# Kernel tuning notes

Hardware: AMD Instinct MI355X
Metric: run time of the kernel (lower is better)

Reference implementation:

```python
import jax, jax.numpy as jnp
import numpy as np
from jax import lax

# Static config (matches init_kwargs)
D_MODEL = 1024
EXPAND = 2
D_INNER = D_MODEL * EXPAND          # 2048
HEAD_DIM = 64
N_HEADS = D_INNER // HEAD_DIM       # 32
N_GROUPS = 1
D_STATE = 128
D_CONV = 4
CONV_DIM = D_INNER + 2 * N_GROUPS * D_STATE        # 2304
D_IN_PROJ = 2 * D_INNER + 2 * N_GROUPS * D_STATE + N_HEADS  # 4384
SEQLEN = 8192
LN_EPS = 1e-5


def setup_inputs() -> dict:
    key = jax.random.key(0)
    ks = jax.random.split(key, 6)
    x = jax.random.normal(ks[0], (SEQLEN, D_MODEL), jnp.float32)
    W_in = jax.random.normal(ks[1], (D_IN_PROJ, D_MODEL), jnp.float32) / np.sqrt(D_MODEL)
    W_conv = jax.random.normal(ks[2], (CONV_DIM, 1, D_CONV), jnp.float32) / np.sqrt(D_CONV)
    b_conv = jnp.zeros((CONV_DIM,), jnp.float32)
    # dt_bias init per Mamba2: dt ~ LogUniform(dt_min, dt_max), inverse-softplus
    dt = jnp.exp(jax.random.uniform(ks[3], (N_HEADS,)) * (np.log(0.1) - np.log(0.001)) + np.log(0.001))
    dt = jnp.clip(dt, 1e-4)
    dt_bias = dt + jnp.log(-jnp.expm1(-dt))
    A_log = jnp.log(jax.random.uniform(ks[4], (N_HEADS,), minval=1.0, maxval=16.0))
    D_param = jnp.ones((N_HEADS,), jnp.float32)
    ln_w = jnp.ones((D_INNER,), jnp.float32)
    ln_b = jnp.zeros((D_INNER,), jnp.float32)
    W_out = jax.random.normal(ks[5], (D_MODEL, D_INNER), jnp.float32) / np.sqrt(D_INNER)
    return dict(x=x, W_in=W_in, W_conv=W_conv, b_conv=b_conv, dt_bias=dt_bias,
                A_log=A_log, D_param=D_param, ln_w=ln_w, ln_b=ln_b, W_out=W_out)


def reference(x, W_in, W_conv, b_conv, dt_bias, A_log, D_param, ln_w, ln_b, W_out):
    L = x.shape[0]
    zxbcdt = x @ W_in.T                                   # (L, d_in_proj)
    z = zxbcdt[:, :D_INNER]                               # gate
    xbc = zxbcdt[:, D_INNER:D_INNER + CONV_DIM]           # (L, conv_dim)
    dt = jax.nn.softplus(zxbcdt[:, D_INNER + CONV_DIM:] + dt_bias)  # (L, h)
    # depthwise causal-window conv with SAME padding over the sequence
    lhs = xbc.T[None]                                      # (1, conv_dim, L)
    conv = lax.conv_general_dilated(lhs, W_conv, (1,), 'SAME',
                                    feature_group_count=CONV_DIM,
                                    dimension_numbers=('NCH', 'OIH', 'NCH'))[0]
    xbc = jax.nn.silu((conv + b_conv[:, None]).T)          # (L, conv_dim)
    x_ssm = xbc[:, :D_INNER].reshape(L, N_HEADS, HEAD_DIM)
    B = xbc[:, D_INNER:D_INNER + N_GROUPS * D_STATE].reshape(L, N_GROUPS, D_STATE)
    C = xbc[:, D_INNER + N_GROUPS * D_STATE:].reshape(L, N_GROUPS, D_STATE)
    hpg = N_HEADS // N_GROUPS
    Bh = jnp.repeat(B, hpg, axis=1)                        # (L, h, n)
    Ch = jnp.repeat(C, hpg, axis=1)                        # (L, h, n)
    A = -jnp.exp(A_log)                                    # (h,), negative
    a = jnp.exp(dt * A)                                    # (L, h) per-token decay in (0,1)
    V = x_ssm * dt[..., None]                              # discretized input (L, h, p)
    # non-causal SSD (VSSD): global state H then readout, plus D skip
    H = jnp.einsum('lhn,lh,lhp->hnp', Bh, a, V)            # (h, n, p)
    y = jnp.einsum('lhn,hnp->lhp', Ch, H) + D_param[None, :, None] * x_ssm
    y = y.reshape(L, D_INNER)
    # LayerNorm (eqx default: weight+bias, eps=1e-5), then gate by z
    mu = jnp.mean(y, axis=-1, keepdims=True)
    var = jnp.var(y, axis=-1, keepdims=True)
    y = ((y - mu) / jnp.sqrt(var + LN_EPS)) * ln_w + ln_b
    y = y * z
    return y @ W_out.T                                     # (L, d_model)
```

## Files before the change

kernel.cpp:

```cpp
#include <hip/hip_runtime.h>
#include <hip/hip_bf16.h>
#include <math.h>

#define L_SEQ 8192
#define DM 1024
#define DI 2048
#define NH 32
#define HD 64
#define DS 128
#define CDIM 2304
#define DPROJ 4384
#define NPAD_IN 4608
#define KSPLIT 16
#define OPROWS 2176

typedef short bf16x8 __attribute__((ext_vector_type(8)));
typedef float floatx4 __attribute__((ext_vector_type(4)));
typedef unsigned short u16x4 __attribute__((ext_vector_type(4)));
typedef unsigned short u16x8 __attribute__((ext_vector_type(8)));

#define AS1(p) ((const __attribute__((address_space(1))) void*)(p))
#define AS3(p) ((__attribute__((address_space(3))) void*)(p))

__device__ __forceinline__ float bf2f(unsigned short u) {
  union { unsigned int i; float f; } c; c.i = ((unsigned int)u) << 16; return c.f;
}
__device__ __forceinline__ unsigned short f2bf(float f) {
  return __bfloat16_as_ushort(__float2bfloat16(f));
}

template <int OMODE>
__global__ __launch_bounds__(512, 4)
void gemm128_tlp(const unsigned short* __restrict__ A, int lda,
                 const unsigned short* __restrict__ B, int ldb,
                 void* __restrict__ Cout, int ldc,
                 int K, int Nstore) {
  __shared__ __align__(16) char lds[65536];
  const int t = threadIdx.x;
  const int lane = t & 63;
  const int w = t >> 6;
  const int wm = w & 1, wn = w >> 1;
  const int fr = lane & 15, quad = lane >> 4;

  int gx = gridDim.x, gy = gridDim.y;
  int linear = blockIdx.y * gx + blockIdx.x;
  int xcd = linear & 7, loc = linear >> 3;
  int mper = gy >> 3;
  int mt = xcd * mper + loc % mper;
  int nt = loc / mper;
  const int m0 = mt << 7, n0 = nt << 7;
  const int NT = K >> 6;

  floatx4 acc[4][2];
#pragma unroll
  for (int i = 0; i < 4; ++i)
#pragma unroll
    for (int j = 0; j < 2; ++j) acc[i][j] = (floatx4){0.f, 0.f, 0.f, 0.f};
  bf16x8 af[4][2], b0[2], b1[2];

  auto stA = [&](int buf, int kt) {
#pragma unroll
    for (int i = 0; i < 2; ++i) {
      int o = (i * 512 + t) * 16;
      int os = o ^ (((o >> 7) & 7) << 4);
      int rloc = os >> 7, kb = os & 127;
      const unsigned short* src = A + (size_t)(m0 + rloc) * lda + (kt << 6) + (kb >> 1);
      __builtin_amdgcn_global_load_lds(AS1(src), AS3(lds + buf * 16384 + o), 16, 0, 0);
    }
  };
  auto stB = [&](int buf, int kt) {
#pragma unroll
    for (int i = 0; i < 2; ++i) {
      int o = (i * 512 + t) * 16;
      int os = o ^ (((o >> 7) & 7) << 4);
      int rloc = os >> 7, kb = os & 127;
      const unsigned short* src = B + (size_t)(n0 + rloc) * ldb + (kt << 6) + (kb >> 1);
      __builtin_amdgcn_global_load_lds(AS1(src),
          AS3(lds + 32768 + buf * 16384 + o), 16, 0, 0);
    }
  };
  auto rdA = [&](int buf, int mi, int ks) -> bf16x8 {
    int rloc = (wm << 6) | (mi << 4) | fr;
    return *(const bf16x8*)(lds + buf * 16384 + rloc * 128 +
                            (((ks << 6) | (quad << 4)) ^ ((fr & 7) << 4)));
  };
  auto rdB = [&](int buf, int ni, int ks) -> bf16x8 {
    int rloc = (wn << 5) | (ni << 4) | fr;
    return *(const bf16x8*)(lds + 32768 + buf * 16384 + rloc * 128 +
                            (((ks << 6) | (quad << 4)) ^ ((fr & 7) << 4)));
  };

  stA(0, 0); stB(0, 0);
  if (NT > 1) {
    stA(1, 1);
    asm volatile("s_waitcnt vmcnt(2)" ::: "memory");
  } else {
    asm volatile("s_waitcnt vmcnt(0)" ::: "memory");
  }
  __builtin_amdgcn_s_barrier();

  for (int kt = 0; kt < NT; ++kt) {
    const int buf = kt & 1;
    const bool pfB = (kt + 1 < NT);
    const bool pfA = (kt + 2 < NT);
#pragma unroll
    for (int mi = 0; mi < 4; ++mi) { af[mi][0] = rdA(buf, mi, 0); af[mi][1] = rdA(buf, mi, 1); }
    b0[0] = rdB(buf, 0, 0); b0[1] = rdB(buf, 0, 1);
    if (pfB) stB(buf ^ 1, kt + 1);
    __builtin_amdgcn_s_barrier();
    asm volatile("s_waitcnt lgkmcnt(0)" ::: "memory");
    __builtin_amdgcn_s_setprio(1);
#pragma unroll
    for (int mi = 0; mi < 4; ++mi)
#pragma unroll
      for (int ks = 0; ks < 2; ++ks)
        acc[mi][0] = __builtin_amdgcn_mfma_f32_16x16x32_bf16(af[mi][ks], b0[ks], acc[mi][0], 0, 0, 0);
    __builtin_amdgcn_s_setprio(0);
    __builtin_amdgcn_s_barrier();
    b1[0] = rdB(buf, 1, 0); b1[1] = rdB(buf, 1, 1);
    if (pfA) stA(buf, kt + 2);
    __builtin_amdgcn_s_barrier();
    asm volatile("s_waitcnt lgkmcnt(0)" ::: "memory");
    __builtin_amdgcn_s_setprio(1);
#pragma unroll
    for (int mi = 0; mi < 4; ++mi)
#pragma unroll
      for (int ks = 0; ks < 2; ++ks)
        acc[mi][1] = __builtin_amdgcn_mfma_f32_16x16x32_bf16(af[mi][ks], b1[ks], acc[mi][1], 0, 0, 0);
    __builtin_amdgcn_s_setprio(0);
    if (kt < NT - 1) {
      if (pfA) asm volatile("s_waitcnt vmcnt(2)" ::: "memory");
      else     asm volatile("s_waitcnt vmcnt(0)" ::: "memory");
      __builtin_amdgcn_s_barrier();
    }
  }

  if (OMODE == 0) {
    __syncthreads();
    unsigned short* rp = (unsigned short*)lds;
    unsigned short* C = (unsigned short*)Cout;
    const int mb = wm * 64, nb = wn * 32;
#pragma unroll
    for (int mi = 0; mi < 4; ++mi)
#pragma unroll
      for (int ni = 0; ni < 2; ++ni)
#pragma unroll
        for (int r = 0; r < 4; ++r)
          rp[(mb + mi * 16 + quad * 4 + r) * 128 + nb + ni * 16 + fr] = f2bf(acc[mi][ni][r]);
    __syncthreads();
#pragma unroll
    for (int j = 0; j < 4; ++j) {
      int lin = j * 4096 + t * 8;
      int row = lin >> 7, col = lin & 127;
      int gcol = n0 + col;
      if (gcol < Nstore)
        *(u16x8*)&C[(size_t)(m0 + row) * ldc + gcol] = *(const u16x8*)&rp[lin];
    }
  } else {
    float* Cf = (float*)Cout;
#pragma unroll
    for (int mi = 0; mi < 4; ++mi)
#pragma unroll
      for (int ni = 0; ni < 2; ++ni) {
        int gcol = n0 + wn * 32 + ni * 16 + fr;
        int grow = m0 + wm * 64 + mi * 16 + quad * 4;
#pragma unroll
        for (int r = 0; r < 4; ++r)
          if (gcol < Nstore)
            Cf[(size_t)(grow + r) * ldc + gcol] = acc[mi][ni][r];
      }
  }
}

template <int MODE>
__global__ __launch_bounds__(256)
void gemm_bt_mfma(const unsigned short* __restrict__ A, int lda,
                  const unsigned short* __restrict__ B, int ldb,
                  void* __restrict__ Cout, int ldc,
                  int Kfull, int Nstore,
                  const unsigned short* __restrict__ xs,
                  const float* __restrict__ Dvec) {
  __shared__ __align__(16) char smem[17408];
  unsigned short* Asm = (unsigned short*)smem;
  unsigned short* Bsm = Asm + 128 * 32;
  const int t = threadIdx.x;

  int bx = blockIdx.x, by = blockIdx.y;
  if (MODE != 2) {
    int gx = gridDim.x;
    int linear = by * gx + bx;
    int xcd = linear & 7;
    int local = linear >> 3;
    by = xcd * 8 + (local & 7);
    bx = local >> 3;
  }
  const int m0 = by * 128;
  const int n0 = bx * 128;

  int kstart = 0, klen = Kfull;
  if (MODE == 2) { klen = Kfull / KSPLIT; kstart = blockIdx.z * klen; }
  const int wave = t >> 6, lane = t & 63;
  const int wm = (wave & 1) * 64;
  const int wn = (wave >> 1) * 64;
  const int fr = lane & 15;
  const int quad = lane >> 4;

  floatx4 acc[4][4];
#pragma unroll
  for (int i = 0; i < 4; ++i)
#pragma unroll
    for (int j = 0; j < 4; ++j) acc[i][j] = (floatx4){0.f, 0.f, 0.f, 0.f};

  for (int k0 = kstart; k0 < kstart + klen; k0 += 32) {
#pragma unroll
    for (int i = 0; i < 2; ++i) {
      int linear = i * 256 + t;
      int row = linear >> 2;
      int kq = (linear & 3) * 8;
      const unsigned short* ga = A + (size_t)(m0 + row) * lda + (k0 + kq);
      const unsigned short* gb = B + (size_t)(n0 + row) * ldb + (k0 + kq);
      __builtin_amdgcn_global_load_lds(AS1(ga), AS3(&Asm[linear * 8]), 16, 0, 0);
      __builtin_amdgcn_global_load_lds(AS1(gb), AS3(&Bsm[linear * 8]), 16, 0, 0);
    }
    __syncthreads();

    bf16x8 af[4], bfr[4];
#pragma unroll
    for (int i = 0; i < 4; ++i) {
      af[i]  = *(const bf16x8*)&Asm[(wm + i * 16 + fr) * 32 + quad * 8];
      bfr[i] = *(const bf16x8*)&Bsm[(wn + i * 16 + fr) * 32 + quad * 8];
    }
#pragma unroll
    for (int mi = 0; mi < 4; ++mi)
#pragma unroll
      for (int ni = 0; ni < 4; ++ni)
        acc[mi][ni] = __builtin_amdgcn_mfma_f32_16x16x32_bf16(
            af[mi], bfr[ni], acc[mi][ni], 0, 0, 0);
    __syncthreads();
  }

  const int lrbase = (wm ? 16 : 0) + quad * 4;
  if (MODE == 0 || MODE == 1) {
    unsigned short(*rp)[136] = (unsigned short(*)[136])smem;
    unsigned short* C = (unsigned short*)Cout;
#pragma unroll
    for (int mi = 0; mi < 4; ++mi) {
      __syncthreads();
#pragma unroll
      for (int ni = 0; ni < 4; ++ni)
#pragma unroll
        for (int r = 0; r < 4; ++r)
          rp[lrbase + r][wn + ni * 16 + fr] = f2bf(acc[mi][ni][r]);
      __syncthreads();
#pragma unroll
      for (int j = 0; j < 2; ++j) {
        int off = j * 2048 + t * 8;
        int lr = off >> 7, c = off & 127;
        int grow = m0 + (lr >> 4) * 64 + mi * 16 + (lr & 15);
        int gcol = n0 + c;
        u16x8 v = *(const u16x8*)&rp[lr][c];
        if (MODE == 1) {
          u16x8 xv = *(const u16x8*)&xs[(size_t)grow * ldc + gcol];
          float Dh = Dvec[gcol >> 6];
          u16x8 o;
#pragma unroll
          for (int e = 0; e < 8; ++e) o[e] = f2bf(bf2f(v[e]) + Dh * bf2f(xv[e]));
          *(u16x8*)&C[(size_t)grow * ldc + gcol] = o;
        } else {
          if (gcol < Nstore) *(u16x8*)&C[(size_t)grow * ldc + gcol] = v;
        }
      }
    }
  } else {
    float(*rpf)[136] = (float(*)[136])smem;
    float* C = (float*)Cout;
    if (MODE == 2) C += (size_t)blockIdx.z * DS * DI;
#pragma unroll
    for (int mi = 0; mi < 4; ++mi) {
      __syncthreads();
#pragma unroll
      for (int ni = 0; ni < 4; ++ni)
#pragma unroll
        for (int r = 0; r < 4; ++r)
          rpf[lrbase + r][wn + ni * 16 + fr] = acc[mi][ni][r];
      __syncthreads();
#pragma unroll
      for (int j = 0; j < 4; ++j) {
        int off = j * 1024 + t * 4;
        int lr = off >> 7, c = off & 127;
        int grow = m0 + (lr >> 4) * 64 + mi * 16 + (lr & 15);
        int gcol = n0 + c;
        float4 v = *(const float4*)&rpf[lr][c];
        *(float4*)&C[(size_t)grow * ldc + gcol] = v;
      }
    }
  }
}

__global__ __launch_bounds__(256)
void cast_all_kernel(const float* __restrict__ x, const float* __restrict__ W_in,
                     const float* __restrict__ W_out,
                     unsigned short* __restrict__ x_bf16,
                     unsigned short* __restrict__ win_bf16,
                     unsigned short* __restrict__ wout_bf16) {
  int b = blockIdx.x;
  int t = threadIdx.x;
  u16x4 o = (u16x4){0, 0, 0, 0};
  if (b < 8192) {
    size_t i4 = ((size_t)b * 256 + t) * 4;
    float4 v = *(const float4*)(x + i4);
    o.x = f2bf(v.x); o.y = f2bf(v.y); o.z = f2bf(v.z); o.w = f2bf(v.w);
    *(u16x4*)(x_bf16 + i4) = o;
  } else if (b < 12800) {
    size_t i4 = ((size_t)(b - 8192) * 256 + t) * 4;
    int row = (int)(i4 >> 10);
    if (row < DPROJ) {
      float4 v = *(const float4*)(W_in + i4);
      o.x = f2bf(v.x); o.y = f2bf(v.y); o.z = f2bf(v.z); o.w = f2bf(v.w);
    }
    *(u16x4*)(win_bf16 + i4) = o;
  } else {
    size_t i4 = ((size_t)(b - 12800) * 256 + t) * 4;
    float4 v = *(const float4*)(W_out + i4);
    o.x = f2bf(v.x); o.y = f2bf(v.y); o.z = f2bf(v.z); o.w = f2bf(v.w);
    *(u16x4*)(wout_bf16 + i4) = o;
  }
}

__global__ __launch_bounds__(256)
void dt_kernel(const unsigned short* __restrict__ zxb, const float* __restrict__ dt_bias,
               const float* __restrict__ A_log, float* __restrict__ s_out) {
  int idx = blockIdx.x * 256 + threadIdx.x;
  int l = idx >> 5, h = idx & 31;
  float v = bf2f(zxb[(size_t)l * DPROJ + (DI + CDIM) + h]) + dt_bias[h];
  float d = (v > 20.f) ? v : log1pf(expf(v));
  s_out[idx] = d * expf(-d * expf(A_log[h]));
}

__global__ __launch_bounds__(256)
void conv_fused_kernel(const unsigned short* __restrict__ zxb,
                       const float* __restrict__ Wc,
                       const float* __restrict__ bc,
                       const float* __restrict__ svec,
                       unsigned short* __restrict__ xs,
                       unsigned short* __restrict__ cb,
                       unsigned short* __restrict__ OpT) {
  __shared__ unsigned short zt[67][66];
  __shared__ unsigned short ot[64][66];
  __shared__ float sl[64];
  const int c0 = blockIdx.x * 64;
  const int l0 = blockIdx.y * 64;
  const int t = threadIdx.x;
  for (int idx = t; idx < 67 * 16; idx += 256) {
    int row = idx >> 4;
    int colq = (idx & 15) * 4;
    int gl = l0 - 1 + row;
    u16x4 v = (u16x4){0, 0, 0, 0};
    if (gl >= 0 && gl < L_SEQ)
      v = *(const u16x4*)&zxb[(size_t)gl * DPROJ + DI + c0 + colq];
    *(u16x4*)&zt[row][colq] = v;
  }
  const bool isX = (c0 < DI);
  const bool isC = (c0 >= DI + DS);
  if (isX && t < 64) sl[t] = svec[(size_t)(l0 + t) * NH + (c0 >> 6)];
  const int c = t & 63;
  const int gc = c0 + c;
  const float4 wv = *(const float4*)&Wc[gc * 4];
  const float bias = bc[gc];
  const int lq = (t >> 6) * 16;
  __syncthreads();
#pragma unroll
  for (int i = 0; i < 16; ++i) {
    int ll = lq + i;
    float sacc = bias + bf2f(zt[ll][c]) * wv.x + bf2f(zt[ll + 1][c]) * wv.y +
                 bf2f(zt[ll + 2][c]) * wv.z + bf2f(zt[ll + 3][c]) * wv.w;
    float v = sacc / (1.f + expf(-sacc));
    int gl = l0 + ll;
    if (isC) {
      cb[(size_t)gl * DS + (gc - (DI + DS))] = f2bf(v);
    } else if (isX) {
      xs[(size_t)gl * DI + gc] = f2bf(v);
      ot[c][ll] = f2bf(v * sl[ll]);
    } else {
      ot[c][ll] = f2bf(v);
    }
  }
  if (!isC) {
    __syncthreads();
#pragma unroll
    for (int j = 0; j < 4; ++j) {
      int linear = j * 1024 + t * 4;
      int rr = linear >> 6;
      int lc = linear & 63;
      *(u16x4*)&OpT[(size_t)(c0 + rr) * L_SEQ + l0 + lc] = *(const u16x4*)&ot[rr][lc];
    }
  }
}

__global__ __launch_bounds__(256)
void h_reduce_t_kernel(const float* __restrict__ P, unsigned short* __restrict__ Ht) {
  __shared__ float tile[32][65];
  const int bid = blockIdx.x;
  const int pt = bid & 31, ng = bid >> 5;
  const int t = threadIdx.x;
#pragma unroll
  for (int i = 0; i < 8; ++i) {
    int nl = i * 4 + (t >> 6);
    int n = ng * 32 + nl;
    int p = pt * 64 + (t & 63);
    float acc = 0.f;
#pragma unroll
    for (int z = 0; z < KSPLIT; ++z)
      acc += P[(size_t)z * (DS * DI) + (size_t)n * DI + p];
    tile[nl][t & 63] = acc;
  }
  __syncthreads();
#pragma unroll
  for (int j = 0; j < 8; ++j) {
    int linear = j * 256 + t;
    int pl = linear >> 5, nl = linear & 31;
    Ht[(size_t)(pt * 64 + pl) * DS + ng * 32 + nl] = f2bf(tile[nl][pl]);
  }
}

__global__ __launch_bounds__(256)
void ln_mul_kernel(const unsigned short* __restrict__ ybuf, unsigned short* __restrict__ zxb,
                   const float* __restrict__ ln_w, const float* __restrict__ ln_b) {
  int l = blockIdx.x;
  int t = threadIdx.x;
  int c0 = t * 8;
  u16x8 yv = *(const u16x8*)&ybuf[(size_t)l * DI + c0];
  float vals[8];
  float s = 0.f, sq = 0.f;
#pragma unroll
  for (int i = 0; i < 8; ++i) {
    float v = bf2f(yv[i]);
    vals[i] = v;
    s += v;
    sq += v * v;
  }
#pragma unroll
  for (int off = 32; off > 0; off >>= 1) {
    s += __shfl_down(s, off, 64);
    sq += __shfl_down(sq, off, 64);
  }
  __shared__ float red[10];
  int wave = t >> 6, lane = t & 63;
  if (lane == 0) { red[wave] = s; red[4 + wave] = sq; }
  __syncthreads();
  if (t == 0) {
    float S = red[0] + red[1] + red[2] + red[3];
    float SQ = red[4] + red[5] + red[6] + red[7];
    float mu = S / (float)DI;
    red[8] = mu;
    red[9] = rsqrtf(SQ / (float)DI - mu * mu + 1e-5f);
  }
  __syncthreads();
  float mu = red[8], rstd = red[9];
  unsigned short* zrow = zxb + (size_t)l * DPROJ;
  u16x8 zv = *(const u16x8*)&zrow[c0];
  float4 w0 = *(const float4*)&ln_w[c0], w1 = *(const float4*)&ln_w[c0 + 4];
  float4 b0 = *(const float4*)&ln_b[c0], b1 = *(const float4*)&ln_b[c0 + 4];
  float w[8] = {w0.x, w0.y, w0.z, w0.w, w1.x, w1.y, w1.z, w1.w};
  float b[8] = {b0.x, b0.y, b0.z, b0.w, b1.x, b1.y, b1.z, b1.w};
  u16x8 o;
#pragma unroll
  for (int i = 0; i < 8; ++i) {
    float v = (vals[i] - mu) * rstd * w[i] + b[i];
    o[i] = f2bf(v * bf2f(zv[i]));
  }
  *(u16x8*)&zrow[DI + c0] = o;
}

extern "C" void kernel_launch(void* const* d_in, const int* in_sizes, int n_in,
                              void* d_out, int out_size, void* d_ws, size_t ws_size,
                              hipStream_t stream) {
  const float* x       = (const float*)d_in[0];
  const float* W_in    = (const float*)d_in[1];
  const float* W_conv  = (const float*)d_in[2];
  const float* b_conv  = (const float*)d_in[3];
  const float* dt_bias = (const float*)d_in[4];
  const float* A_log   = (const float*)d_in[5];
  const float* D_param = (const float*)d_in[6];
  const float* ln_w    = (const float*)d_in[7];
  const float* ln_b    = (const float*)d_in[8];
  const float* W_out   = (const float*)d_in[9];
  float* out = (float*)d_out;

  unsigned short* zxb = (unsigned short*)d_ws;
  unsigned short* xs   = zxb + (size_t)L_SEQ * DPROJ;
  unsigned short* cb   = xs + (size_t)L_SEQ * DI;
  float* svec = (float*)(cb + (size_t)L_SEQ * DS);
  unsigned short* OpT = (unsigned short*)(svec + (size_t)L_SEQ * NH);
  float* Ppart = (float*)(OpT + (size_t)OPROWS * L_SEQ);
  unsigned short* Ht = (unsigned short*)(Ppart + (size_t)KSPLIT * DS * DI);
  unsigned short* wout_bf16 = Ht + (size_t)DI * DS;
  unsigned short* x_bf16   = OpT;
  unsigned short* win_bf16 = OpT + (size_t)L_SEQ * DM;
  unsigned short* ybuf     = OpT;

  cast_all_kernel<<<14848, 256, 0, stream>>>(x, W_in, W_out, x_bf16, win_bf16,
                                             wout_bf16);

  gemm128_tlp<0><<<dim3(NPAD_IN / 128, L_SEQ / 128), 512, 0, stream>>>(
      x_bf16, DM, win_bf16, DM, zxb, DPROJ, DM, DPROJ);

  dt_kernel<<<(L_SEQ * NH) / 256, 256, 0, stream>>>(zxb, dt_bias, A_log, svec);

  conv_fused_kernel<<<dim3(CDIM / 64, L_SEQ / 64), 256, 0, stream>>>(
      zxb, W_conv, b_conv, svec, xs, cb, OpT);

  gemm_bt_mfma<2><<<dim3(DI / 128, 1, KSPLIT), 256, 0, stream>>>(
      OpT + (size_t)DI * L_SEQ, L_SEQ, OpT, L_SEQ, Ppart, DI, L_SEQ, DI,
      nullptr, nullptr);

  h_reduce_t_kernel<<<128, 256, 0, stream>>>(Ppart, Ht);

  gemm_bt_mfma<1><<<dim3(DI / 128, L_SEQ / 128), 256, 0, stream>>>(
      cb, DS, Ht, DS, ybuf, DI, DS, DI, xs, D_param);

  ln_mul_kernel<<<L_SEQ, 256, 0, stream>>>(ybuf, zxb, ln_w, ln_b);

  gemm128_tlp<1><<<dim3(DM / 128, L_SEQ / 128), 512, 0, stream>>>(
      zxb + DI, DPROJ, wout_bf16, DI, out, DM, DI, DM);
}
```

Baseline: 323.9 us.

## Restructure 128x128 GEMM into triple-buffered K=32 pipeline with fewer barriers

Rewrites the main bf16 GEMM to use a K-step of 32 with a three-slot LDS ring buffer, prefetching two steps ahead. Each iteration now has a single barrier instead of three. LDS drops to 48KB and launch bounds rise to allow more resident blocks. The cost is twice as many iterations, each with less MFMA work, and the XOR swizzle on LDS reads is removed, which may cause bank conflicts.

Measured after the change: 344.1 us. 1.06x slower.

```diff
diff --git a/kernel.cpp b/kernel.cpp
--- a/kernel.cpp
+++ b/kernel.cpp
@@ -30,12 +30,12 @@
 }
 
 template <int OMODE>
-__global__ __launch_bounds__(512, 4)
-void gemm128_tlp(const unsigned short* __restrict__ A, int lda,
-                 const unsigned short* __restrict__ B, int ldb,
-                 void* __restrict__ Cout, int ldc,
-                 int K, int Nstore) {
-  __shared__ __align__(16) char lds[65536];
+__global__ __launch_bounds__(512, 6)
+void gemm128_tlp3(const unsigned short* __restrict__ A, int lda,
+                  const unsigned short* __restrict__ B, int ldb,
+                  void* __restrict__ Cout, int ldc,
+                  int K, int Nstore) {
+  __shared__ __align__(16) char lds[49152];
   const int t = threadIdx.x;
   const int lane = t & 63;
   const int w = t >> 6;
@@ -49,90 +49,69 @@
   int mt = xcd * mper + loc % mper;
   int nt = loc / mper;
   const int m0 = mt << 7, n0 = nt << 7;
-  const int NT = K >> 6;
+  const int NT = K >> 5;
 
   floatx4 acc[4][2];
 #pragma unroll
   for (int i = 0; i < 4; ++i)
 #pragma unroll
     for (int j = 0; j < 2; ++j) acc[i][j] = (floatx4){0.f, 0.f, 0.f, 0.f};
-  bf16x8 af[4][2], b0[2], b1[2];
-
-  auto stA = [&](int buf, int kt) {
-#pragma unroll
-    for (int i = 0; i < 2; ++i) {
-      int o = (i * 512 + t) * 16;
-      int os = o ^ (((o >> 7) & 7) << 4);
-      int rloc = os >> 7, kb = os & 127;
-      const unsigned short* src = A + (size_t)(m0 + rloc) * lda + (kt << 6) + (kb >> 1);
-      __builtin_amdgcn_global_load_lds(AS1(src), AS3(lds + buf * 16384 + o), 16, 0, 0);
-    }
+  bf16x8 af[4], bb[2];
+
+  auto stA = [&](int slot, int kt) {
+    int o = t * 16;
+    int rloc = o >> 6, kb = o & 63;
+    const unsigned short* src = A + (size_t)(m0 + rloc) * lda + (kt << 5) + (kb >> 1);
+    __builtin_amdgcn_global_load_lds(AS1(src), AS3(lds + slot * 16384 + o), 16, 0, 0);
   };
-  auto stB = [&](int buf, int kt) {
-#pragma unroll
-    for (int i = 0; i < 2; ++i) {
-      int o = (i * 512 + t) * 16;
-      int os = o ^ (((o >> 7) & 7) << 4);
-      int rloc = os >> 7, kb = os & 127;
-      const unsigned short* src = B + (size_t)(n0 + rloc) * ldb + (kt << 6) + (kb >> 1);
-      __builtin_amdgcn_global_load_lds(AS1(src),
-          AS3(lds + 32768 + buf * 16384 + o), 16, 0, 0);
-    }
+  auto stB = [&](int slot, int kt) {
+    int o = t * 16;
+    int rloc = o >> 6, kb = o & 63;
+    const unsigned short* src = B + (size_t)(n0 + rloc) * ldb + (kt << 5) + (kb >> 1);
+    __builtin_amdgcn_global_load_lds(AS1(src), AS3(lds + slot * 16384 + 8192 + o), 16, 0, 0);
   };
-  auto rdA = [&](int buf, int mi, int ks) -> bf16x8 {
+  auto rdA = [&](int slot, int mi) -> bf16x8 {
     int rloc = (wm << 6) | (mi << 4) | fr;
-    return *(const bf16x8*)(lds + buf * 16384 + rloc * 128 +
-                            (((ks << 6) | (quad << 4)) ^ ((fr & 7) << 4)));
+    return *(const bf16x8*)(lds + slot * 16384 + rloc * 64 + quad * 16);
   };
-  auto rdB = [&](int buf, int ni, int ks) -> bf16x8 {
+  auto rdB = [&](int slot, int ni) -> bf16x8 {
     int rloc = (wn << 5) | (ni << 4) | fr;
-    return *(const bf16x8*)(lds + 32768 + buf * 16384 + rloc * 128 +
-                            (((ks << 6) | (quad << 4)) ^ ((fr & 7) << 4)));
+    return *(const bf16x8*)(lds + slot * 16384 + 8192 + rloc * 64 + quad * 16);
   };
 
   stA(0, 0); stB(0, 0);
   if (NT > 1) {
-    stA(1, 1);
+    stA(1, 1); stB(1, 1);
     asm volatile("s_waitcnt vmcnt(2)" ::: "memory");
   } else {
     asm volatile("s_waitcnt vmcnt(0)" ::: "memory");
   }
   __builtin_amdgcn_s_barrier();
 
+  int cur = 0;
   for (int kt = 0; kt < NT; ++kt) {
-    const int buf = kt & 1;
-    const bool pfB = (kt + 1 < NT);
-    const bool pfA = (kt + 2 < NT);
-#pragma unroll
-    for (int mi = 0; mi < 4; ++mi) { af[mi][0] = rdA(buf, mi, 0); af[mi][1] = rdA(buf, mi, 1); }
-    b0[0] = rdB(buf, 0, 0); b0[1] = rdB(buf, 0, 1);
-    if (pfB) stB(buf ^ 1, kt + 1);
-    __builtin_amdgcn_s_barrier();
+    const bool pf = (kt + 2 < NT);
+#pragma unroll
+    for (int mi = 0; mi < 4; ++mi) af[mi] = rdA(cur, mi);
+    bb[0] = rdB(cur, 0); bb[1] = rdB(cur, 1);
+    if (pf) {
+      int s2 = cur + 2; if (s2 >= 3) s2 -= 3;
+      stA(s2, kt + 2); stB(s2, kt + 2);
+    }
     asm volatile("s_waitcnt lgkmcnt(0)" ::: "memory");
     __builtin_amdgcn_s_setprio(1);
 #pragma unroll
-    for (int mi = 0; mi < 4; ++mi)
-#pragma unroll
-      for (int ks = 0; ks < 2; ++ks)
-        acc[mi][0] = __builtin_amdgcn_mfma_f32_16x16x32_bf16(af[mi][ks], b0[ks], acc[mi][0], 0, 0, 0);
-    __builtin_amdgcn_s_setprio(0);
-    __builtin_amdgcn_s_barrier();
-    b1[0] = rdB(buf, 1, 0); b1[1] = rdB(buf, 1, 1);
-    if (pfA) stA(buf, kt + 2);
-    __builtin_amdgcn_s_barrier();
-    asm volatile("s_waitcnt lgkmcnt(0)" ::: "memory");
-    __builtin_amdgcn_s_setprio(1);
-#pragma unroll
-    for (int mi = 0; mi < 4; ++mi)
-#pragma unroll
-      for (int ks = 0; ks < 2; ++ks)
-        acc[mi][1] = __builtin_amdgcn_mfma_f32_16x16x32_bf16(af[mi][ks], b1[ks], acc[mi][1], 0, 0, 0);
+    for (int mi = 0; mi < 4; ++mi) {
+      acc[mi][0] = __builtin_amdgcn_mfma_f32_16x16x32_bf16(af[mi], bb[0], acc[mi][0], 0, 0, 0);
+      acc[mi][1] = __builtin_amdgcn_mfma_f32_16x16x32_bf16(af[mi], bb[1], acc[mi][1], 0, 0, 0);
+    }
     __builtin_amdgcn_s_setprio(0);
     if (kt < NT - 1) {
-      if (pfA) asm volatile("s_waitcnt vmcnt(2)" ::: "memory");
-      else     asm volatile("s_waitcnt vmcnt(0)" ::: "memory");
+      if (pf) asm volatile("s_waitcnt vmcnt(2)" ::: "memory");
+      else    asm volatile("s_waitcnt vmcnt(0)" ::: "memory");
       __builtin_amdgcn_s_barrier();
     }
+    ++cur; if (cur == 3) cur = 0;
   }
 
   if (OMODE == 0) {
@@ -502,7 +481,7 @@
   cast_all_kernel<<<14848, 256, 0, stream>>>(x, W_in, W_out, x_bf16, win_bf16,
                                              wout_bf16);
 
-  gemm128_tlp<0><<<dim3(NPAD_IN / 128, L_SEQ / 128), 512, 0, stream>>>(
+  gemm128_tlp3<0><<<dim3(NPAD_IN / 128, L_SEQ / 128), 512, 0, stream>>>(
       x_bf16, DM, win_bf16, DM, zxb, DPROJ, DM, DPROJ);
 
   dt_kernel<<<(L_SEQ * NH) / 256, 256, 0, stream>>>(zxb, dt_bias, A_log, svec);
@@ -521,6 +500,6 @@
 
   ln_mul_kernel<<<L_SEQ, 256, 0, stream>>>(ybuf, zxb, ln_w, ln_b);
 
-  gemm128_tlp<1><<<dim3(DM / 128, L_SEQ / 128), 512, 0, stream>>>(
+  gemm128_tlp3<1><<<dim3(DM / 128, L_SEQ / 128), 512, 0, stream>>>(
       zxb + DI, DPROJ, wout_bf16, DI, out, DM, DI, DM);
 }
```
